# Performance work log

Measured on AMD Instinct MI355X. Metric: run time of the kernel, lower is better.

The kernel has to match this reference:

```python
import jax, jax.numpy as jnp
import numpy as np

HIDDEN = 2048
NUM_V = 16
NUM_K = 8
HK = 128
HV = 128
KCONV = 4
KEY_DIM = NUM_K * HK      # 1024
VALUE_DIM = NUM_V * HV    # 2048
CONV_DIM = 2 * KEY_DIM + VALUE_DIM  # 4096
R = NUM_V // NUM_K        # 2
L2_EPS = 1e-6
NORM_EPS = 1e-6


def setup_inputs() -> dict:
    key = jax.random.key(0)
    ks = jax.random.split(key, 8)
    s = 0.02
    return {
        "hidden_states": jax.random.normal(ks[0], (1, 1024, HIDDEN), jnp.float32),
        "w_qkvz": jax.random.normal(ks[1], (2 * KEY_DIM + 2 * VALUE_DIM, HIDDEN), jnp.float32) * s,
        "w_ba": jax.random.normal(ks[2], (2 * NUM_V, HIDDEN), jnp.float32) * s,
        "conv_w": jax.random.normal(ks[3], (CONV_DIM, KCONV), jnp.float32) * s,
        "dt_bias": jnp.ones((NUM_V,), jnp.float32),
        "A_log": jnp.log(jax.random.uniform(ks[4], (NUM_V,), jnp.float32, 1e-3, 16.0)),
        "norm_weight": jnp.ones((HV,), jnp.float32),
        "w_out": jax.random.normal(ks[5], (HIDDEN, VALUE_DIM), jnp.float32) * s,
    }


def reference(hidden_states, w_qkvz, w_ba, conv_w, dt_bias, A_log, norm_weight, w_out):
    B, T, _ = hidden_states.shape
    # --- input projections ---
    qkvz = hidden_states @ w_qkvz.T                     # [B,T,2K+2V]
    ba = hidden_states @ w_ba.T                         # [B,T,2*Hv]
    # fix_query_key_value_ordering: group by k-head, layout [hk, hk, r*hv, r*hv]
    qkvz = qkvz.reshape(B, T, NUM_K, 2 * HK + 2 * R * HV)
    q, k, v, z = jnp.split(qkvz, [HK, 2 * HK, 2 * HK + R * HV], axis=3)
    v = v.reshape(B, T, NUM_V, HV)
    z = z.reshape(B, T, NUM_V, HV)
    ba = ba.reshape(B, T, NUM_K, 2 * R)
    b = ba[..., :R].reshape(B, T, NUM_V)
    a = ba[..., R:].reshape(B, T, NUM_V)
    # --- depthwise causal conv1d + silu over concatenated q,k,v ---
    mixed = jnp.concatenate(
        [q.reshape(B, T, KEY_DIM), k.reshape(B, T, KEY_DIM), v.reshape(B, T, VALUE_DIM)], axis=-1
    )
    xc = mixed.transpose(0, 2, 1)                       # [B,C,T]
    yc = jax.lax.conv_general_dilated(
        xc, conv_w[:, None, :], (1,), [(KCONV - 1, 0)],
        feature_group_count=CONV_DIM, dimension_numbers=("NCH", "OIH", "NCH"),
    )
    yc = jax.nn.silu(yc).transpose(0, 2, 1)             # [B,T,C]
    q, k, v = jnp.split(yc, [KEY_DIM, 2 * KEY_DIM], axis=-1)
    q = q.reshape(B, T, NUM_K, HK)
    k = k.reshape(B, T, NUM_K, HK)
    v = v.reshape(B, T, NUM_V, HV)
    # --- gates ---
    beta = jax.nn.sigmoid(b)                            # [B,T,Hv]
    g = -jnp.exp(A_log) * jax.nn.softplus(a + dt_bias)  # [B,T,Hv] (log decay, <=0)
    # GQA expansion of q,k to value heads
    q = jnp.repeat(q, R, axis=2)                        # [B,T,Hv,hk]
    k = jnp.repeat(k, R, axis=2)
    # l2 norm on q,k (use_qk_l2norm_in_kernel=True)
    q = q * jax.lax.rsqrt(jnp.sum(q * q, -1, keepdims=True) + L2_EPS)
    k = k * jax.lax.rsqrt(jnp.sum(k * k, -1, keepdims=True) + L2_EPS)
    scale = HK ** -0.5
    # --- gated delta rule recurrence ---
    def step(S, xs):
        qt, kt, vt, gt, bt = xs                          # per-timestep slices
        S = S * jnp.exp(gt)[..., None, None]             # decay state [B,Hv,hk,hv]
        kv = jnp.einsum("bhk,bhkv->bhv", kt, S)          # readout at k_t
        delta = (vt - kv) * bt[..., None]                # beta-gated delta
        S = S + jnp.einsum("bhk,bhv->bhkv", kt, delta)
        o = jnp.einsum("bhk,bhkv->bhv", qt * scale, S)
        return S, o

    S0 = jnp.zeros((B, NUM_V, HK, HV), hidden_states.dtype)
    xs = (
        q.transpose(1, 0, 2, 3), k.transpose(1, 0, 2, 3), v.transpose(1, 0, 2, 3),
        g.transpose(1, 0, 2), beta.transpose(1, 0, 2),
    )
    _, o = jax.lax.scan(step, S0, xs)                   # o: [T,B,Hv,hv]
    o = o.transpose(1, 0, 2, 3)                         # [B,T,Hv,hv]
    # --- gated RMSNorm (gate applied before normalization, Mamba2/Qwen3Next style) ---
    xf = o.astype(jnp.float32) * jax.nn.silu(z.astype(jnp.float32))
    var = jnp.mean(xf * xf, -1, keepdims=True)
    xn = xf * jax.lax.rsqrt(var + NORM_EPS) * norm_weight
    # --- output projection ---
    return xn.reshape(B, T, VALUE_DIM) @ w_out.T
```

## Files before the change

### kernel.cpp

```cpp
#include <hip/hip_runtime.h>
#include <math.h>

#define T_LEN   1024
#define HIDDEN  2048
#define QKVZ_N  6144
#define VAL_DIM 2048

typedef _Float16 half8 __attribute__((ext_vector_type(8)));
typedef _Float16 half4 __attribute__((ext_vector_type(4)));
typedef _Float16 half2t __attribute__((ext_vector_type(2)));
typedef float floatx4 __attribute__((ext_vector_type(4)));

__device__ __forceinline__ float sigmoidf_(float x) { return 1.f / (1.f + expf(-x)); }

__device__ __forceinline__ void gl_lds16(const _Float16* g, _Float16* l) {
    __builtin_amdgcn_global_load_lds(
        (const __attribute__((address_space(1))) void*)g,
        (__attribute__((address_space(3))) void*)l, 16, 0, 0);
}

__global__ __launch_bounds__(256) void cvt3(const float* __restrict__ s0, _Float16* __restrict__ d0, int n0,
                                            const float* __restrict__ s1, _Float16* __restrict__ d1, int n1,
                                            const float* __restrict__ s2, _Float16* __restrict__ d2, int n2) {
    int i = blockIdx.x * 256 + threadIdx.x;
    const float* s;
    _Float16* d;
    if (i < n0) { s = s0; d = d0; }
    else if (i < n0 + n1) { s = s1; d = d1; i -= n0; }
    else if (i < n0 + n1 + n2) { s = s2; d = d2; i -= n0 + n1; }
    else return;
    const float4 v = ((const float4*)s)[i];
    half4 h;
    h[0] = (_Float16)v.x; h[1] = (_Float16)v.y;
    h[2] = (_Float16)v.z; h[3] = (_Float16)v.w;
    *(half4*)&d[i * 4] = h;
}

template <typename OutT>
__global__ __launch_bounds__(256, 2) void gemm_h16(const _Float16* __restrict__ A,
                                                   const _Float16* __restrict__ W,
                                                   OutT* __restrict__ C,
                                                   int MB, int NB, int K) {
    const int N = NB * 128;
    const int l = blockIdx.x;
    const int x = l & 7;
    const int tt = l >> 3;
    const int mb = tt % MB;
    const int nb = x + 8 * (tt / MB);
    const int m0 = mb * 64, n0 = nb * 128;

    const int t = threadIdx.x;
    const int wave = t >> 6;
    const int lane = t & 63;
    const int wr = (wave >> 1) * 32;
    const int wc = (wave & 1) * 64;
    const int l15 = lane & 15;
    const int quad = lane >> 4;
    const int srow = lane >> 3;
    const int slot = lane & 7;

    __shared__ __align__(16) _Float16 Ah[2][4096];
    __shared__ __align__(16) _Float16 Bh[2][8192];

    floatx4 acc[2][4];
#pragma unroll
    for (int i = 0; i < 2; ++i)
#pragma unroll
        for (int j = 0; j < 4; ++j) acc[i][j] = 0;

    auto stage = [&](int buf, int k0) {
#pragma unroll
        for (int g = 0; g < 2; ++g) {
            const int r = wave * 16 + g * 8 + srow;
            const int kc = slot ^ (r & 7);
            gl_lds16(A + (size_t)(m0 + r) * K + k0 + kc * 8,
                     &Ah[buf][(wave * 128 + g * 64) * 8]);
        }
#pragma unroll
        for (int g = 0; g < 4; ++g) {
            const int r = wave * 32 + g * 8 + srow;
            const int kc = slot ^ (r & 7);
            gl_lds16(W + (size_t)(n0 + r) * K + k0 + kc * 8,
                     &Bh[buf][(wave * 256 + g * 64) * 8]);
        }
    };

    const int NIT = K >> 6;
    stage(0, 0);
    __syncthreads();
    int cur = 0;
    for (int it = 0; it < NIT; ++it) {
        if (it + 1 < NIT) stage(cur ^ 1, (it + 1) * 64);
        half8 af[2][2], bf[4][2];
#pragma unroll
        for (int mt = 0; mt < 2; ++mt)
#pragma unroll
            for (int ks = 0; ks < 2; ++ks) {
                const int m = wr + mt * 16 + l15;
                const int kq = ks * 4 + quad;
                af[mt][ks] = *(const half8*)&Ah[cur][(m * 8 + (kq ^ (m & 7))) * 8];
            }
#pragma unroll
        for (int nt = 0; nt < 4; ++nt)
#pragma unroll
            for (int ks = 0; ks < 2; ++ks) {
                const int n = wc + nt * 16 + l15;
                const int kq = ks * 4 + quad;
                bf[nt][ks] = *(const half8*)&Bh[cur][(n * 8 + (kq ^ (n & 7))) * 8];
            }
#pragma unroll
        for (int mt = 0; mt < 2; ++mt)
#pragma unroll
            for (int nt = 0; nt < 4; ++nt)
#pragma unroll
                for (int ks = 0; ks < 2; ++ks)
                    acc[mt][nt] = __builtin_amdgcn_mfma_f32_16x16x32_f16(
                        af[mt][ks], bf[nt][ks], acc[mt][nt], 0, 0, 0);
        if (it + 1 < NIT) {
            __syncthreads();
            cur ^= 1;
        }
    }
#pragma unroll
    for (int mt = 0; mt < 2; ++mt)
#pragma unroll
        for (int nt = 0; nt < 4; ++nt) {
            const int c = n0 + wc + nt * 16 + l15;
#pragma unroll
            for (int reg = 0; reg < 4; ++reg) {
                const int r = m0 + wr + mt * 16 + quad * 4 + reg;
                C[(size_t)r * N + c] = (OutT)acc[mt][nt][reg];
            }
        }
}

__global__ __launch_bounds__(256) void gemm_ba_gates(const float* __restrict__ A,
                                                     const float* __restrict__ W,
                                                     const float* __restrict__ dt_bias,
                                                     const float* __restrict__ A_log,
                                                     float* __restrict__ lgd,
                                                     float* __restrict__ bet) {
    const int m = blockIdx.x;
    const int tid = threadIdx.x;
    const int kl = tid & 31;
    const int ng = tid >> 5;
    const float* Arow = A + (size_t)m * 2048;
    __shared__ float sba[32];

    float4 a4[16];
#pragma unroll
    for (int j = 0; j < 16; ++j)
        a4[j] = *(const float4*)(Arow + j * 128 + kl * 4);

#pragma unroll
    for (int nn = 0; nn < 4; ++nn) {
        const int n = nn * 8 + ng;
        const float* Wrow = W + (size_t)n * 2048;
        float acc = 0.f;
#pragma unroll
        for (int j = 0; j < 16; ++j) {
            const float4 w4 = *(const float4*)(Wrow + j * 128 + kl * 4);
            acc = fmaf(a4[j].x, w4.x, acc);
            acc = fmaf(a4[j].y, w4.y, acc);
            acc = fmaf(a4[j].z, w4.z, acc);
            acc = fmaf(a4[j].w, w4.w, acc);
        }
        acc += __shfl_xor(acc, 1, 64);
        acc += __shfl_xor(acc, 2, 64);
        acc += __shfl_xor(acc, 4, 64);
        acc += __shfl_xor(acc, 8, 64);
        acc += __shfl_xor(acc, 16, 64);
        if (kl == 0) sba[n] = acc;
    }
    __syncthreads();
    if (tid < 16) {
        const int vh = tid, kh = vh >> 1, r = vh & 1;
        const float b = sba[kh * 4 + r];
        const float a = sba[kh * 4 + 2 + r];
        bet[m * 16 + vh] = 1.f / (1.f + expf(-b));
        const float xx = a + dt_bias[vh];
        const float sp = (xx > 0.f) ? (xx + log1pf(expf(-xx))) : log1pf(expf(xx));
        lgd[m * 16 + vh] = -expf(A_log[vh]) * sp;
    }
}

__global__ __launch_bounds__(512) void conv_silu_l2(const _Float16* __restrict__ qkvz,
                                                    const float* __restrict__ conv_w,
                                                    _Float16* __restrict__ qc,
                                                    _Float16* __restrict__ kc,
                                                    _Float16* __restrict__ vc) {
    const int t = blockIdx.x;
    const int c = threadIdx.x * 8;
    int col;
    _Float16* dst;
    bool isqk;
    float extra = 1.f;
    if (c < 1024) {
        col = ((c >> 7) * 768) + (c & 127);
        dst = qc + t * 1024 + c;
        isqk = true;
        extra = 0.08838834764831845f;
    } else if (c < 2048) {
        const int cc = c - 1024;
        col = ((cc >> 7) * 768) + 128 + (cc & 127);
        dst = kc + t * 1024 + cc;
        isqk = true;
    } else {
        const int cc = c - 2048;
        col = ((cc >> 8) * 768) + 256 + (cc & 255);
        dst = vc + (size_t)t * 2048 + cc;
        isqk = false;
    }
    const size_t gb = (size_t)t * QKVZ_N + col;
    const half8 x3 = *(const half8*)(qkvz + gb);
    half8 x2, x1, x0;
    if (t >= 1) x2 = *(const half8*)(qkvz + gb - QKVZ_N);
    if (t >= 2) x1 = *(const half8*)(qkvz + gb - 2 * (size_t)QKVZ_N);
    if (t >= 3) x0 = *(const half8*)(qkvz + gb - 3 * (size_t)QKVZ_N);

    float y[8];
    float ss = 0.f;
#pragma unroll
    for (int u = 0; u < 8; ++u) {
        const float4 wv = *(const float4*)(conv_w + (c + u) * 4);
        float acc = (float)x3[u] * wv.w;
        if (t >= 1) acc = fmaf((float)x2[u], wv.z, acc);
        if (t >= 2) acc = fmaf((float)x1[u], wv.y, acc);
        if (t >= 3) acc = fmaf((float)x0[u], wv.x, acc);
        acc = acc * (1.f / (1.f + expf(-acc)));
        y[u] = acc;
        ss = fmaf(acc, acc, ss);
    }
    half8 ov;
    if (isqk) {
        ss += __shfl_xor(ss, 1, 64);
        ss += __shfl_xor(ss, 2, 64);
        ss += __shfl_xor(ss, 4, 64);
        ss += __shfl_xor(ss, 8, 64);
        const float r = rsqrtf(ss + 1e-6f) * extra;
#pragma unroll
        for (int u = 0; u < 8; ++u) ov[u] = (_Float16)(y[u] * r);
    } else {
#pragma unroll
        for (int u = 0; u < 8; ++u) ov[u] = (_Float16)y[u];
    }
    *(half8*)dst = ov;
}

__global__ __launch_bounds__(256) void chunk_prep(
    const _Float16* __restrict__ qch, const _Float16* __restrict__ kch,
    const _Float16* __restrict__ vch, const float* __restrict__ lgd,
    const float* __restrict__ bet, _Float16* __restrict__ CH,
    float* __restrict__ gamC) {
    const int blk = blockIdx.x;
    const int c = blk >> 4, h = blk & 15, kh = h >> 1;
    const int c0 = c * 64;
    const int tid = threadIdx.x, lane = tid & 63, wave = tid >> 6;
    const int l15 = lane & 15, quad = lane >> 4;

    __shared__ __align__(16) _Float16 Ksh[8192];
    __shared__ __align__(16) _Float16 Qsh[8192];
    __shared__ float Amat[64 * 65];
    __shared__ float Gs[64], Bets[64], Gam[64];

    {
        const int t = tid >> 2, kc0 = (tid & 3) * 4;
        const size_t gb = (size_t)(c0 + t) * 1024 + kh * 128;
#pragma unroll
        for (int i = 0; i < 4; ++i) {
            const int kc = kc0 + i;
            half8 kv = *(const half8*)(kch + gb + kc * 8);
            half8 qv = *(const half8*)(qch + gb + kc * 8);
            const int chl = t * 16 + (kc ^ (t & 15));
            *(half8*)&Ksh[chl * 8] = kv;
            *(half8*)&Qsh[chl * 8] = qv;
        }
    }
    if (tid < 64) {
        float g = lgd[(size_t)(c0 + tid) * 16 + h];
#pragma unroll
        for (int off = 1; off < 64; off <<= 1) {
            float y = __shfl_up(g, off, 64);
            if (tid >= off) g += y;
        }
        Gs[tid] = g;
        Gam[tid] = expf(g);
        Bets[tid] = bet[(size_t)(c0 + tid) * 16 + h];
    }
    __syncthreads();

    _Float16* CHb = CH + (size_t)(c * 16 + h) * 36864;
    _Float16* Ug = CHb;
    _Float16* Wtg = CHb + 8192;
    _Float16* Khg = CHb + 16384;
    _Float16* Qgg = CHb + 24576;
    _Float16* Lg = CHb + 32768;

    {
        floatx4 accKK[4], accQK[4];
#pragma unroll
        for (int tt = 0; tt < 4; ++tt) { accKK[tt] = 0; accQK[tt] = 0; }
        half8 bfK[4];
#pragma unroll
        for (int ks = 0; ks < 4; ++ks) {
            const int i = wave * 16 + l15;
            const int kc = ks * 4 + quad;
            bfK[ks] = *(const half8*)&Ksh[(i * 16 + (kc ^ (i & 15))) * 8];
        }
#pragma unroll
        for (int tt = 0; tt < 4; ++tt) {
            const int t = tt * 16 + l15;
#pragma unroll
            for (int ks = 0; ks < 4; ++ks) {
                const int kc = ks * 4 + quad;
                const int chl = (t * 16 + (kc ^ (t & 15))) * 8;
                half8 afK = *(const half8*)&Ksh[chl];
                half8 afQ = *(const half8*)&Qsh[chl];
                accKK[tt] = __builtin_amdgcn_mfma_f32_16x16x32_f16(afK, bfK[ks], accKK[tt], 0, 0, 0);
                accQK[tt] = __builtin_amdgcn_mfma_f32_16x16x32_f16(afQ, bfK[ks], accQK[tt], 0, 0, 0);
            }
        }
        const int ii = wave * 16 + l15;
        const float Gi = Gs[ii];
#pragma unroll
        for (int tt = 0; tt < 4; ++tt)
#pragma unroll
            for (int r = 0; r < 4; ++r) {
                const int t = tt * 16 + quad * 4 + r;
                const float Gt = Gs[t];
                const float ratio = (ii <= t) ? expf(Gt - Gi) : 0.f;
                if (ii < t) Amat[t * 65 + ii] = Bets[t] * ratio * accKK[tt][r];
                Lg[t * 64 + ii] = (_Float16)((ii <= t) ? ratio * accQK[tt][r] : 0.f);
            }
    }
    __syncthreads();

    {
        const int j = tid;
        float x[64];
        if (j < 128) {
#pragma unroll
            for (int t = 0; t < 64; ++t)
                x[t] = Bets[t] * (float)vch[(size_t)(c0 + t) * 2048 + h * 128 + j];
        } else {
            const int k = j - 128;
#pragma unroll
            for (int t = 0; t < 64; ++t) {
                const int chl = t * 16 + ((k >> 3) ^ (t & 15));
                x[t] = Bets[t] * Gam[t] * (float)Ksh[chl * 8 + (k & 7)];
            }
        }
#pragma unroll
        for (int t = 1; t < 64; ++t) {
            float acc = 0.f;
#pragma unroll
            for (int i = 0; i < t; ++i) acc = fmaf(Amat[t * 65 + i], x[i], acc);
            x[t] -= acc;
        }
        if (j < 128) {
#pragma unroll
            for (int t = 0; t < 64; t += 4) {
                half4 w4;
                w4[0] = (_Float16)x[t]; w4[1] = (_Float16)x[t + 1];
                w4[2] = (_Float16)x[t + 2]; w4[3] = (_Float16)x[t + 3];
                *(half4*)&Wtg[j * 64 + t] = w4;
            }
        } else {
            const int k = j - 128;
#pragma unroll
            for (int t = 0; t < 64; ++t) Ug[t * 128 + k] = (_Float16)x[t];
        }
    }

    {
        const float g63 = Gs[63];
        const int k = tid >> 1, cb = (tid & 1) * 32;
#pragma unroll
        for (int cc = 0; cc < 32; cc += 4) {
            half4 o4;
#pragma unroll
            for (int u = 0; u < 4; ++u) {
                const int ci = cb + cc + u;
                const int chl = ci * 16 + ((k >> 3) ^ (ci & 15));
                o4[u] = (_Float16)(expf(g63 - Gs[ci]) * (float)Ksh[chl * 8 + (k & 7)]);
            }
            *(half4*)&Khg[k * 64 + cb + cc] = o4;
        }
        const int cq = tid >> 2, kb = (tid & 3) * 4;
        const float gam = Gam[cq];
#pragma unroll
        for (int kc = 0; kc < 4; ++kc) {
            const int kcc = kb + kc;
            half8 q8 = *(const half8*)&Qsh[(cq * 16 + (kcc ^ (cq & 15))) * 8];
            half8 s8;
#pragma unroll
            for (int u = 0; u < 8; ++u) s8[u] = (_Float16)(gam * (float)q8[u]);
            *(half8*)&Qgg[cq * 128 + kcc * 8] = s8;
        }
        if (tid == 0) gamC[c * 16 + h] = Gam[63];
    }
}

struct ScanOps {
    half8 aU[4];
    half8 aQ[4];
    half8 aL[2];
    half8 aK[2][2];
    half4 wv;
    float gC;
};

__global__ __launch_bounds__(256) void chunk_scan(const _Float16* __restrict__ CH,
                                                  const float* __restrict__ gamC,
                                                  float* __restrict__ o) {
    const int h = blockIdx.x & 15;
    const int vsl = blockIdx.x >> 4;
    const int tid = threadIdx.x, lane = tid & 63, wave = tid >> 6;
    const int l15 = lane & 15, quad = lane >> 4;
    const int tw = wave * 16;
    const int kw = wave * 32;
    const int sKey = l15 << 1;
    const int dKey = (l15 << 1) & 14;

    __shared__ __align__(16) _Float16 Ssh[16 * 128];
    __shared__ __align__(16) _Float16 Dsh[16 * 64];

    *(half8*)&Ssh[tid * 8] = half8{0, 0, 0, 0, 0, 0, 0, 0};
    floatx4 Sacc[2];
    Sacc[0] = 0; Sacc[1] = 0;
    __syncthreads();

    auto loadOps = [&](ScanOps& S, int c) {
        const _Float16* CHb = CH + (size_t)(c * 16 + h) * 36864;
#pragma unroll
        for (int ks = 0; ks < 4; ++ks) {
            S.aU[ks] = *(const half8*)(CHb + (tw + l15) * 128 + ks * 32 + quad * 8);
            S.aQ[ks] = *(const half8*)(CHb + 24576 + (tw + l15) * 128 + ks * 32 + quad * 8);
        }
#pragma unroll
        for (int cs = 0; cs < 2; ++cs) {
            S.aL[cs] = *(const half8*)(CHb + 32768 + (tw + l15) * 64 + cs * 32 + quad * 8);
#pragma unroll
            for (int kt = 0; kt < 2; ++kt)
                S.aK[kt][cs] = *(const half8*)(CHb + 16384 + (kw + kt * 16 + l15) * 64 + cs * 32 + quad * 8);
        }
        S.wv = *(const half4*)(CHb + 8192 + (vsl * 16 + l15) * 64 + tw + quad * 4);
        S.gC = gamC[c * 16 + h];
    };

    auto chunkBody = [&](const ScanOps& S, int c) {
        half8 bs[4];
#pragma unroll
        for (int ks = 0; ks < 4; ++ks)
            bs[ks] = *(const half8*)&Ssh[(l15 * 32 + ((ks * 8 + quad * 2) ^ sKey)) * 4];
        floatx4 xa = {0.f, 0.f, 0.f, 0.f};
#pragma unroll
        for (int ks = 0; ks < 4; ++ks)
            xa = __builtin_amdgcn_mfma_f32_16x16x32_f16(S.aU[ks], bs[ks], xa, 0, 0, 0);
        half4 d4;
#pragma unroll
        for (int r = 0; r < 4; ++r) d4[r] = (_Float16)((float)S.wv[r] - xa[r]);
        *(half4*)&Dsh[(l15 * 16 + ((wave * 4 + quad) ^ dKey)) * 4] = d4;
        __syncthreads();

        half8 bd[2];
#pragma unroll
        for (int cs = 0; cs < 2; ++cs)
            bd[cs] = *(const half8*)&Dsh[(l15 * 16 + ((cs * 8 + quad * 2) ^ dKey)) * 4];
        floatx4 oacc = {0.f, 0.f, 0.f, 0.f};
#pragma unroll
        for (int ks = 0; ks < 4; ++ks)
            oacc = __builtin_amdgcn_mfma_f32_16x16x32_f16(S.aQ[ks], bs[ks], oacc, 0, 0, 0);
#pragma unroll
        for (int cs = 0; cs < 2; ++cs)
            oacc = __builtin_amdgcn_mfma_f32_16x16x32_f16(S.aL[cs], bd[cs], oacc, 0, 0, 0);
#pragma unroll
        for (int kt = 0; kt < 2; ++kt) {
#pragma unroll
            for (int r = 0; r < 4; ++r) Sacc[kt][r] *= S.gC;
#pragma unroll
            for (int cs = 0; cs < 2; ++cs)
                Sacc[kt] = __builtin_amdgcn_mfma_f32_16x16x32_f16(S.aK[kt][cs], bd[cs], Sacc[kt], 0, 0, 0);
        }
        const int col = h * 128 + vsl * 16 + l15;
#pragma unroll
        for (int r = 0; r < 4; ++r)
            o[(size_t)(c * 64 + tw + quad * 4 + r) * 2048 + col] = oacc[r];
#pragma unroll
        for (int kt = 0; kt < 2; ++kt) {
            half4 s4;
#pragma unroll
            for (int r = 0; r < 4; ++r) s4[r] = (_Float16)Sacc[kt][r];
            *(half4*)&Ssh[(l15 * 32 + ((wave * 8 + kt * 4 + quad) ^ sKey)) * 4] = s4;
        }
        __syncthreads();
    };

    ScanOps A_, B_;
    loadOps(A_, 0);
#pragma unroll 1
    for (int cc = 0; cc < 16; cc += 2) {
        loadOps(B_, cc + 1);
        chunkBody(A_, cc);
        if (cc + 2 < 16) loadOps(A_, cc + 2);
        chunkBody(B_, cc + 1);
    }
}

__global__ __launch_bounds__(64) void gated_norm(const float* __restrict__ o,
                                                 const _Float16* __restrict__ qkvz,
                                                 const float* __restrict__ nw,
                                                 _Float16* __restrict__ xn) {
    const int b = blockIdx.x;
    const int t = b >> 4;
    const int vh = b & 15;
    const int kh = vh >> 1;
    const int r = vh & 1;
    const float* op = o + (size_t)t * 2048 + vh * 128;
    const _Float16* zp = qkvz + (size_t)t * QKVZ_N + kh * 768 + 512 + r * 128;
    const int j = threadIdx.x * 2;
    const float2 ov = *(const float2*)(op + j);
    const half2t zv = *(const half2t*)(zp + j);
    const float z0 = (float)zv[0], z1 = (float)zv[1];
    const float f0 = ov.x * z0 / (1.f + expf(-z0));
    const float f1 = ov.y * z1 / (1.f + expf(-z1));
    float ss = f0 * f0 + f1 * f1;
#pragma unroll
    for (int m = 1; m < 64; m <<= 1) ss += __shfl_xor(ss, m, 64);
    const float rs = rsqrtf(ss * (1.f / 128.f) + 1e-6f);
    _Float16* xp = xn + (size_t)t * 2048 + vh * 128;
    half2t y;
    y[0] = (_Float16)(f0 * rs * nw[j]);
    y[1] = (_Float16)(f1 * rs * nw[j + 1]);
    *(half2t*)(xp + j) = y;
}

extern "C" void kernel_launch(void* const* d_in, const int* in_sizes, int n_in,
                              void* d_out, int out_size, void* d_ws, size_t ws_size,
                              hipStream_t stream) {
    const float* hidden  = (const float*)d_in[0];
    const float* w_qkvz  = (const float*)d_in[1];
    const float* w_ba    = (const float*)d_in[2];
    const float* conv_w  = (const float*)d_in[3];
    const float* dt_bias = (const float*)d_in[4];
    const float* A_log   = (const float*)d_in[5];
    const float* norm_w  = (const float*)d_in[6];
    const float* w_out   = (const float*)d_in[7];
    float* out = (float*)d_out;

    char* w = (char*)d_ws;
    _Float16*  qkvz_h = (_Float16*)(w);
    _Float16*  qch    = (_Float16*)(w + 12713984);
    _Float16*  kch    = (_Float16*)(w + 14811136);
    _Float16*  vch    = (_Float16*)(w + 16908288);
    float*     lgd    = (float*)(w + 21102592);
    float*     bet    = (float*)(w + 21168128);
    float*     gamC   = (float*)(w + 21233664);
    float*     o      = (float*)(w + 21237760);
    _Float16*  hid_h  = (_Float16*)(w + 21237760);
    _Float16*  wqk_h  = (_Float16*)(w + 29626368);
    _Float16*  CH     = (_Float16*)(w + 29626368);
    _Float16*  xn_h   = (_Float16*)(w + 29626368 + 18874368);
    _Float16*  wout_h = (_Float16*)(w + 54792192);

    const int n0 = HIDDEN * T_LEN / 4;
    const int n1 = QKVZ_N * HIDDEN / 4;
    const int n2 = VAL_DIM * HIDDEN / 4;
    cvt3<<<(n0 + n1 + n2 + 255) / 256, 256, 0, stream>>>(hidden, hid_h, n0,
                                                         w_qkvz, wqk_h, n1,
                                                         w_out, wout_h, n2);

    gemm_h16<_Float16><<<16 * 48, 256, 0, stream>>>(hid_h, wqk_h, qkvz_h, 16, 48, HIDDEN);
    gemm_ba_gates<<<T_LEN, 256, 0, stream>>>(hidden, w_ba, dt_bias, A_log, lgd, bet);
    conv_silu_l2<<<T_LEN, 512, 0, stream>>>(qkvz_h, conv_w, qch, kch, vch);
    chunk_prep<<<256, 256, 0, stream>>>(qch, kch, vch, lgd, bet, CH, gamC);
    chunk_scan<<<128, 256, 0, stream>>>(CH, gamC, o);
    gated_norm<<<T_LEN * 16, 64, 0, stream>>>(o, qkvz_h, norm_w, xn_h);
    gemm_h16<float><<<16 * 16, 256, 0, stream>>>(xn_h, wout_h, out, 16, 16, HIDDEN);
}
```

Measured before the change: 286.8 us.

## Deepen GEMM pipeline to 4-stage K32 buffers and fuse hidden-state conversion

The fp16 GEMM switches from a double-buffered K=64 loop to a 4-deep ring of K=32 LDS buffers. Explicit vmcnt waits let two stages stay in flight across a single barrier, and the LDS swizzle is changed to match. The tile width is now a template parameter, so the output projection uses 64-wide N tiles, giving 512 blocks instead of 256. The hidden-state fp32 to fp16 conversion moves into the ba/gates kernel, which already loads those rows, removing one pass from the convert kernel. This trades extra barriers per K step and more partial-tile overhead for better latency hiding and occupancy.

```diff
diff --git a/kernel.cpp b/kernel.cpp
--- a/kernel.cpp
+++ b/kernel.cpp
@@ -19,15 +19,13 @@
         (__attribute__((address_space(3))) void*)l, 16, 0, 0);
 }
 
-__global__ __launch_bounds__(256) void cvt3(const float* __restrict__ s0, _Float16* __restrict__ d0, int n0,
-                                            const float* __restrict__ s1, _Float16* __restrict__ d1, int n1,
+__global__ __launch_bounds__(256) void cvt2(const float* __restrict__ s1, _Float16* __restrict__ d1, int n1,
                                             const float* __restrict__ s2, _Float16* __restrict__ d2, int n2) {
     int i = blockIdx.x * 256 + threadIdx.x;
     const float* s;
     _Float16* d;
-    if (i < n0) { s = s0; d = d0; }
-    else if (i < n0 + n1) { s = s1; d = d1; i -= n0; }
-    else if (i < n0 + n1 + n2) { s = s2; d = d2; i -= n0 + n1; }
+    if (i < n1) { s = s1; d = d1; }
+    else if (i < n1 + n2) { s = s2; d = d2; i -= n1; }
     else return;
     const float4 v = ((const float4*)s)[i];
     half4 h;
@@ -36,95 +34,102 @@
     *(half4*)&d[i * 4] = h;
 }
 
-template <typename OutT>
+template <int NT, typename OutT>
 __global__ __launch_bounds__(256, 2) void gemm_h16(const _Float16* __restrict__ A,
                                                    const _Float16* __restrict__ W,
                                                    OutT* __restrict__ C,
                                                    int MB, int NB, int K) {
-    const int N = NB * 128;
+    const int BN = NT * 32;
+    const int N = NB * BN;
     const int l = blockIdx.x;
     const int x = l & 7;
     const int tt = l >> 3;
     const int mb = tt % MB;
     const int nb = x + 8 * (tt / MB);
-    const int m0 = mb * 64, n0 = nb * 128;
+    const int m0 = mb * 64, n0 = nb * BN;
 
     const int t = threadIdx.x;
     const int wave = t >> 6;
     const int lane = t & 63;
     const int wr = (wave >> 1) * 32;
-    const int wc = (wave & 1) * 64;
+    const int wc = (wave & 1) * (NT * 16);
     const int l15 = lane & 15;
     const int quad = lane >> 4;
-    const int srow = lane >> 3;
-    const int slot = lane & 7;
-
-    __shared__ __align__(16) _Float16 Ah[2][4096];
-    __shared__ __align__(16) _Float16 Bh[2][8192];
-
-    floatx4 acc[2][4];
+
+    __shared__ __align__(16) _Float16 Ah[4][64 * 32];
+    __shared__ __align__(16) _Float16 Bh[4][BN * 32];
+
+    const int Rl = lane >> 2, sl = lane & 3;
+
+    floatx4 acc[2][NT];
 #pragma unroll
     for (int i = 0; i < 2; ++i)
 #pragma unroll
-        for (int j = 0; j < 4; ++j) acc[i][j] = 0;
+        for (int j = 0; j < NT; ++j) acc[i][j] = 0;
 
     auto stage = [&](int buf, int k0) {
-#pragma unroll
-        for (int g = 0; g < 2; ++g) {
-            const int r = wave * 16 + g * 8 + srow;
-            const int kc = slot ^ (r & 7);
-            gl_lds16(A + (size_t)(m0 + r) * K + k0 + kc * 8,
-                     &Ah[buf][(wave * 128 + g * 64) * 8]);
-        }
-#pragma unroll
-        for (int g = 0; g < 4; ++g) {
-            const int r = wave * 32 + g * 8 + srow;
-            const int kc = slot ^ (r & 7);
-            gl_lds16(W + (size_t)(n0 + r) * K + k0 + kc * 8,
-                     &Bh[buf][(wave * 256 + g * 64) * 8]);
+        {
+            const int R = wave * 16 + Rl;
+            const int r = R ^ ((R >> 2) & 1);
+            const int kq = sl ^ (r & 3);
+            gl_lds16(A + (size_t)(m0 + r) * K + k0 + kq * 8,
+                     &Ah[buf][wave * 512]);
+        }
+#pragma unroll
+        for (int g = 0; g < NT / 2; ++g) {
+            const int R = wave * (NT * 8) + g * 16 + Rl;
+            const int r = R ^ ((R >> 2) & 1);
+            const int kq = sl ^ (r & 3);
+            gl_lds16(W + (size_t)(n0 + r) * K + k0 + kq * 8,
+                     &Bh[buf][(wave * (NT / 2) + g) * 512]);
         }
     };
 
-    const int NIT = K >> 6;
+    auto compute = [&](int buf) {
+        half8 af[2], bf[NT];
+#pragma unroll
+        for (int mt = 0; mt < 2; ++mt) {
+            const int m = wr + mt * 16 + l15;
+            const int P = (m * 4 + (quad ^ (m & 3))) ^ (m & 4);
+            af[mt] = *(const half8*)&Ah[buf][P * 8];
+        }
+#pragma unroll
+        for (int nt = 0; nt < NT; ++nt) {
+            const int n = wc + nt * 16 + l15;
+            const int P = (n * 4 + (quad ^ (n & 3))) ^ (n & 4);
+            bf[nt] = *(const half8*)&Bh[buf][P * 8];
+        }
+#pragma unroll
+        for (int mt = 0; mt < 2; ++mt)
+#pragma unroll
+            for (int nt = 0; nt < NT; ++nt)
+                acc[mt][nt] = __builtin_amdgcn_mfma_f32_16x16x32_f16(
+                    af[mt], bf[nt], acc[mt][nt], 0, 0, 0);
+    };
+
+    const int NIT = K >> 5;
     stage(0, 0);
-    __syncthreads();
-    int cur = 0;
-    for (int it = 0; it < NIT; ++it) {
-        if (it + 1 < NIT) stage(cur ^ 1, (it + 1) * 64);
-        half8 af[2][2], bf[4][2];
-#pragma unroll
-        for (int mt = 0; mt < 2; ++mt)
-#pragma unroll
-            for (int ks = 0; ks < 2; ++ks) {
-                const int m = wr + mt * 16 + l15;
-                const int kq = ks * 4 + quad;
-                af[mt][ks] = *(const half8*)&Ah[cur][(m * 8 + (kq ^ (m & 7))) * 8];
-            }
-#pragma unroll
-        for (int nt = 0; nt < 4; ++nt)
-#pragma unroll
-            for (int ks = 0; ks < 2; ++ks) {
-                const int n = wc + nt * 16 + l15;
-                const int kq = ks * 4 + quad;
-                bf[nt][ks] = *(const half8*)&Bh[cur][(n * 8 + (kq ^ (n & 7))) * 8];
-            }
-#pragma unroll
-        for (int mt = 0; mt < 2; ++mt)
-#pragma unroll
-            for (int nt = 0; nt < 4; ++nt)
-#pragma unroll
-                for (int ks = 0; ks < 2; ++ks)
-                    acc[mt][nt] = __builtin_amdgcn_mfma_f32_16x16x32_f16(
-                        af[mt][ks], bf[nt][ks], acc[mt][nt], 0, 0, 0);
-        if (it + 1 < NIT) {
-            __syncthreads();
-            cur ^= 1;
-        }
-    }
+    stage(1, 32);
+    if constexpr (NT == 4) asm volatile("s_waitcnt vmcnt(3)" ::: "memory");
+    else                   asm volatile("s_waitcnt vmcnt(2)" ::: "memory");
+    __builtin_amdgcn_s_barrier();
+
+    for (int it = 0; it < NIT - 2; ++it) {
+        stage((it + 2) & 3, (it + 2) * 32);
+        compute(it & 3);
+        if constexpr (NT == 4) asm volatile("s_waitcnt vmcnt(3)" ::: "memory");
+        else                   asm volatile("s_waitcnt vmcnt(2)" ::: "memory");
+        __builtin_amdgcn_s_barrier();
+    }
+    compute((NIT - 2) & 3);
+    asm volatile("s_waitcnt vmcnt(0)" ::: "memory");
+    __builtin_amdgcn_s_barrier();
+    compute((NIT - 1) & 3);
+
 #pragma unroll
     for (int mt = 0; mt < 2; ++mt)
 #pragma unroll
-        for (int nt = 0; nt < 4; ++nt) {
+        for (int nt = 0; nt < NT; ++nt) {
             const int c = n0 + wc + nt * 16 + l15;
 #pragma unroll
             for (int reg = 0; reg < 4; ++reg) {
@@ -139,7 +144,8 @@
                                                      const float* __restrict__ dt_bias,
                                                      const float* __restrict__ A_log,
                                                      float* __restrict__ lgd,
-                                                     float* __restrict__ bet) {
+                                                     float* __restrict__ bet,
+                                                     _Float16* __restrict__ hid_h) {
     const int m = blockIdx.x;
     const int tid = threadIdx.x;
     const int kl = tid & 31;
@@ -151,6 +157,16 @@
 #pragma unroll
     for (int j = 0; j < 16; ++j)
         a4[j] = *(const float4*)(Arow + j * 128 + kl * 4);
+
+    if (ng == 0) {
+#pragma unroll
+        for (int j = 0; j < 16; ++j) {
+            half4 h;
+            h[0] = (_Float16)a4[j].x; h[1] = (_Float16)a4[j].y;
+            h[2] = (_Float16)a4[j].z; h[3] = (_Float16)a4[j].w;
+            *(half4*)&hid_h[(size_t)m * 2048 + j * 128 + kl * 4] = h;
+        }
+    }
 
 #pragma unroll
     for (int nn = 0; nn < 4; ++nn) {
@@ -563,18 +579,16 @@
     _Float16*  xn_h   = (_Float16*)(w + 29626368 + 18874368);
     _Float16*  wout_h = (_Float16*)(w + 54792192);
 
-    const int n0 = HIDDEN * T_LEN / 4;
     const int n1 = QKVZ_N * HIDDEN / 4;
     const int n2 = VAL_DIM * HIDDEN / 4;
-    cvt3<<<(n0 + n1 + n2 + 255) / 256, 256, 0, stream>>>(hidden, hid_h, n0,
-                                                         w_qkvz, wqk_h, n1,
-                                                         w_out, wout_h, n2);
-
-    gemm_h16<_Float16><<<16 * 48, 256, 0, stream>>>(hid_h, wqk_h, qkvz_h, 16, 48, HIDDEN);
-    gemm_ba_gates<<<T_LEN, 256, 0, stream>>>(hidden, w_ba, dt_bias, A_log, lgd, bet);
+    cvt2<<<(n1 + n2 + 255) / 256, 256, 0, stream>>>(w_qkvz, wqk_h, n1,
+                                                    w_out, wout_h, n2);
+    gemm_ba_gates<<<T_LEN, 256, 0, stream>>>(hidden, w_ba, dt_bias, A_log,
+                                             lgd, bet, hid_h);
+    gemm_h16<4, _Float16><<<16 * 48, 256, 0, stream>>>(hid_h, wqk_h, qkvz_h, 16, 48, HIDDEN);
     conv_silu_l2<<<T_LEN, 512, 0, stream>>>(qkvz_h, conv_w, qch, kch, vch);
     chunk_prep<<<256, 256, 0, stream>>>(qch, kch, vch, lgd, bet, CH, gamC);
     chunk_scan<<<128, 256, 0, stream>>>(CH, gamC, o);
     gated_norm<<<T_LEN * 16, 64, 0, stream>>>(o, qkvz_h, norm_w, xn_h);
-    gemm_h16<float><<<16 * 16, 256, 0, stream>>>(xn_h, wout_h, out, 16, 16, HIDDEN);
-}
+    gemm_h16<2, float><<<16 * 32, 256, 0, stream>>>(xn_h, wout_h, out, 16, 32, HIDDEN);
+}
```

After: 294.4 us. 2.6% more time.
